# Kernel tuning notes

Measured on AMD Instinct MI355X. Metric: run time of the kernel, lower is better.

Reference implementation:

```python
import jax, jax.numpy as jnp
import numpy as np

N_NODES = 100000
N_EDGES = 800000
D = 64
N_ITERS = 3  # n_layers - 1


def setup_inputs() -> dict:
    key = jax.random.key(0)
    k1, k2, k3, k4 = jax.random.split(key, 4)
    x = jax.random.normal(k1, (N_NODES, D), dtype=jnp.float32)
    edge_index = jax.random.randint(k2, (2, N_EDGES), 0, N_NODES, dtype=jnp.int64)
    edge_weight = jax.random.uniform(k3, (N_EDGES,), dtype=jnp.float32)
    # Linear(64, 64) weight, scaled ~ kaiming so 3 stacked layers stay bounded
    W = jax.random.normal(k4, (D, D), dtype=jnp.float32) * (1.0 / np.sqrt(D))
    b = jnp.zeros((D,), dtype=jnp.float32)
    return {"x": x, "edge_index": edge_index, "edge_weight": edge_weight, "W": W, "b": b}


def reference(x, edge_index, edge_weight, W, b):
    # Faithful math of RPINetEncoder.forward: (n_layers-1) iterations of
    # LinearAggregation (weighted scatter-add message passing + shared Linear)
    # followed by ReLU. Dropout output is discarded in the original -> no-op.
    src = edge_index[0]
    dst = edge_index[1]
    n = x.shape[0]
    for _ in range(N_ITERS):
        msgs = edge_weight[:, None] * x[src]                      # [E, D] gather
        agg = jax.ops.segment_sum(msgs, dst, num_segments=n)      # [N, D] scatter-add
        x = jax.nn.relu(agg @ W.T + b)                            # shared linear + relu
    return x
```

## Files before the change

kernel.cpp:

```cpp
#include <hip/hip_runtime.h>
#include <hip/hip_bf16.h>

#define D 64
#define FP_SCALE 1048576.0f
#define FP_INV   (1.0f / 1048576.0f)

__global__ void hist_kernel(const int* __restrict__ dst, int* __restrict__ counts, int E) {
    int e = blockIdx.x * blockDim.x + threadIdx.x;
    if (e < E) atomicAdd(&counts[dst[e]], 1);
}

__global__ void alloc_kernel(int* __restrict__ counts_cursor, int2* __restrict__ seg,
                             int* __restrict__ total, int N) {
    int n = blockIdx.x * blockDim.x + threadIdx.x;
    if (n < N) {
        int c = counts_cursor[n];
        int s = atomicAdd(total, c);
        seg[n] = make_int2(s, c);
        counts_cursor[n] = s;
    }
}

__global__ void fill_kernel(const int* __restrict__ src, const int* __restrict__ dst,
                            const float* __restrict__ ew, int* __restrict__ cursor,
                            float2* __restrict__ perm, int E) {
    int e = blockIdx.x * blockDim.x + threadIdx.x;
    if (e < E) {
        int p = atomicAdd(&cursor[dst[e]], 1);
        perm[p] = make_float2(__int_as_float(src[e]), ew[e]);
    }
}

__global__ void gather_linear_kernel(const float* __restrict__ x,
                                     const float2* __restrict__ perm,
                                     const int2* __restrict__ seg,
                                     const float* __restrict__ W,
                                     const float* __restrict__ bias,
                                     float* __restrict__ out, int N) {
    __shared__ float Ws[D][D + 1];
    __shared__ float bs[D];
    int t = threadIdx.x;
    for (int i = t; i < D * D; i += 256) Ws[i >> 6][i & 63] = W[i];
    if (t < D) bs[t] = bias[t];
    __syncthreads();

    int wave = t >> 6;
    int lane = t & 63;
    int g = lane >> 4;
    int c = (lane & 15) << 2;
    int nwaves = gridDim.x * 4;
    for (int n = blockIdx.x * 4 + wave; n < N; n += nwaves) {
        int2 sc = seg[n];
        int st = sc.x, cnt = sc.y;
        int ix = 0, iy = 0, iz = 0, iw = 0;
        int k = g;
        for (; k + 4 < cnt; k += 8) {
            float2 m0 = perm[st + k];
            float2 m1 = perm[st + k + 4];
            int s0 = __float_as_int(m0.x);
            int s1 = __float_as_int(m1.x);
            float w0 = m0.y * FP_SCALE;
            float w1 = m1.y * FP_SCALE;
            float4 v0 = *reinterpret_cast<const float4*>(&x[(size_t)s0 * D + c]);
            float4 v1 = *reinterpret_cast<const float4*>(&x[(size_t)s1 * D + c]);
            ix += (int)(w0 * v0.x) + (int)(w1 * v1.x);
            iy += (int)(w0 * v0.y) + (int)(w1 * v1.y);
            iz += (int)(w0 * v0.z) + (int)(w1 * v1.z);
            iw += (int)(w0 * v0.w) + (int)(w1 * v1.w);
        }
        if (k < cnt) {
            float2 m0 = perm[st + k];
            int s0 = __float_as_int(m0.x);
            float w0 = m0.y * FP_SCALE;
            float4 v0 = *reinterpret_cast<const float4*>(&x[(size_t)s0 * D + c]);
            ix += (int)(w0 * v0.x);
            iy += (int)(w0 * v0.y);
            iz += (int)(w0 * v0.z);
            iw += (int)(w0 * v0.w);
        }
        #pragma unroll
        for (int mask = 16; mask <= 32; mask <<= 1) {
            ix += __shfl_xor(ix, mask);
            iy += __shfl_xor(iy, mask);
            iz += __shfl_xor(iz, mask);
            iw += __shfl_xor(iw, mask);
        }
        float ax = (float)ix * FP_INV;
        float ay = (float)iy * FP_INV;
        float az = (float)iz * FP_INV;
        float aw = (float)iw * FP_INV;
        float o = bs[lane];
        #pragma unroll
        for (int d = 0; d < D; ++d) {
            float comp = ((d & 3) == 0) ? ax : ((d & 3) == 1) ? ay : ((d & 3) == 2) ? az : aw;
            float a = __int_as_float(__builtin_amdgcn_readlane(__float_as_int(comp), d >> 2));
            o = fmaf(a, Ws[lane][d], o);
        }
        out[(size_t)n * D + lane] = fmaxf(o, 0.0f);
    }
}

__global__ void rpi_scatter_kernel(const float* __restrict__ x,
                                   const int* __restrict__ src,
                                   const int* __restrict__ dst,
                                   const float* __restrict__ ew,
                                   int* __restrict__ agg, int E) {
    int tid = blockIdx.x * blockDim.x + threadIdx.x;
    int e = tid >> 4;
    if (e >= E) return;
    int c = (tid & 15) << 2;
    int s = src[e], d = dst[e];
    float w = ew[e] * FP_SCALE;
    float4 v = *reinterpret_cast<const float4*>(&x[(size_t)s * D + c]);
    int* o = &agg[(size_t)d * D + c];
    atomicAdd(o + 0, (int)(w * v.x));
    atomicAdd(o + 1, (int)(w * v.y));
    atomicAdd(o + 2, (int)(w * v.z));
    atomicAdd(o + 3, (int)(w * v.w));
}

__global__ void rpi_linear_relu_kernel(const int* __restrict__ agg,
                                       const float* __restrict__ W,
                                       const float* __restrict__ b,
                                       float* __restrict__ out, int N) {
    __shared__ float Ws[D][D + 1];
    __shared__ float bs[D];
    int t = threadIdx.x;
    for (int i = t; i < D * D; i += 256) Ws[i >> 6][i & 63] = W[i];
    if (t < D) bs[t] = b[t];
    __syncthreads();
    int wave = t >> 6, lane = t & 63;
    int nwaves = gridDim.x * 4;
    for (int n = blockIdx.x * 4 + wave; n < N; n += nwaves) {
        const int* arow = &agg[(size_t)n * D];
        float acc = bs[lane];
        #pragma unroll
        for (int d = 0; d < D; ++d) acc = fmaf((float)arow[d] * FP_INV, Ws[lane][d], acc);
        out[(size_t)n * D + lane] = fmaxf(acc, 0.0f);
    }
}

extern "C" void kernel_launch(void* const* d_in, const int* in_sizes, int n_in,
                              void* d_out, int out_size, void* d_ws, size_t ws_size,
                              hipStream_t stream) {
    const float* x0 = (const float*)d_in[0];
    const int*   ei = (const int*)d_in[1];
    const float* ew = (const float*)d_in[2];
    const float* W  = (const float*)d_in[3];
    const float* b  = (const float*)d_in[4];
    float* out = (float*)d_out;

    int N = in_sizes[0] / D;
    int E = in_sizes[2];
    const int* src = ei;
    const int* dst = ei + E;

    size_t xbytes   = (size_t)N * D * sizeof(float);
    size_t intBytes = ((size_t)3 * N + 2) * sizeof(int);
    size_t need     = xbytes + intBytes + (size_t)E * sizeof(float2);

    if (ws_size >= need) {
        float*  xbuf   = (float*)d_ws;
        int2*   seg    = (int2*)((char*)d_ws + xbytes);
        int*    cursor = (int*)(seg + N);
        float2* perm   = (float2*)((char*)d_ws + xbytes + intBytes);
        int*    total  = cursor + N;

        hipMemsetAsync(cursor, 0, (size_t)(N + 2) * sizeof(int), stream);
        int eb = (E + 255) / 256;
        int nb = (N + 255) / 256;
        hist_kernel <<<eb, 256, 0, stream>>>(dst, cursor, E);
        alloc_kernel<<<nb, 256, 0, stream>>>(cursor, seg, total, N);
        fill_kernel <<<eb, 256, 0, stream>>>(src, dst, ew, cursor, perm, E);

        gather_linear_kernel<<<4096, 256, 0, stream>>>(x0,   perm, seg, W, b, out,  N);
        gather_linear_kernel<<<4096, 256, 0, stream>>>(out,  perm, seg, W, b, xbuf, N);
        gather_linear_kernel<<<4096, 256, 0, stream>>>(xbuf, perm, seg, W, b, out,  N);
    } else {
        int* agg = (int*)d_ws;
        const float* xcur = x0;
        int sb = (E * 16 + 255) / 256;
        for (int it = 0; it < 3; ++it) {
            hipMemsetAsync(agg, 0, xbytes, stream);
            rpi_scatter_kernel<<<sb, 256, 0, stream>>>(xcur, src, dst, ew, agg, E);
            rpi_linear_relu_kernel<<<2048, 256, 0, stream>>>(agg, W, b, out, N);
            xcur = out;
        }
    }
}
```

Baseline: 372.4 us.

## Store node features in bf16 for gathers and use a wave-scan CSR offset allocation

Converts the input features to bf16 and keeps the intermediate layer outputs in bf16, which halves the bytes read by the random gathers in each layer. Also pre-scales the edge weights when the CSR is filled, replaces the per-node atomic offset allocation with a wave prefix scan plus one atomic per wave, and splits the matvec accumulation into four independent chains. The cost is an extra conversion kernel, reduced feature precision, and a smaller fixed-point scale that shifts accumulation error.

```diff
diff --git a/kernel.cpp b/kernel.cpp
--- a/kernel.cpp
+++ b/kernel.cpp
@@ -2,8 +2,14 @@
 #include <hip/hip_bf16.h>
 
 #define D 64
-#define FP_SCALE 1048576.0f
-#define FP_INV   (1.0f / 1048576.0f)
+#define FP_SCALE 262144.0f
+#define FP_INV   (1.0f / 262144.0f)
+
+__device__ __forceinline__ unsigned short f2bf(float f) {
+    unsigned int u = __float_as_uint(f);
+    u += 0x7fffu + ((u >> 16) & 1u);
+    return (unsigned short)(u >> 16);
+}
 
 __global__ void hist_kernel(const int* __restrict__ dst, int* __restrict__ counts, int E) {
     int e = blockIdx.x * blockDim.x + threadIdx.x;
@@ -13,11 +19,22 @@
 __global__ void alloc_kernel(int* __restrict__ counts_cursor, int2* __restrict__ seg,
                              int* __restrict__ total, int N) {
     int n = blockIdx.x * blockDim.x + threadIdx.x;
+    int lane = threadIdx.x & 63;
+    int c = (n < N) ? counts_cursor[n] : 0;
+    int incl = c;
+    #pragma unroll
+    for (int off = 1; off < 64; off <<= 1) {
+        int t = __shfl_up(incl, off);
+        if (lane >= off) incl += t;
+    }
+    int wsum = __shfl(incl, 63);
+    int base = 0;
+    if (lane == 63) base = atomicAdd(total, wsum);
+    base = __shfl(base, 63);
     if (n < N) {
-        int c = counts_cursor[n];
-        int s = atomicAdd(total, c);
-        seg[n] = make_int2(s, c);
-        counts_cursor[n] = s;
+        int st = base + incl - c;
+        seg[n] = make_int2(st, c);
+        counts_cursor[n] = st;
     }
 }
 
@@ -27,16 +44,26 @@
     int e = blockIdx.x * blockDim.x + threadIdx.x;
     if (e < E) {
         int p = atomicAdd(&cursor[dst[e]], 1);
-        perm[p] = make_float2(__int_as_float(src[e]), ew[e]);
-    }
-}
-
-__global__ void gather_linear_kernel(const float* __restrict__ x,
+        perm[p] = make_float2(__int_as_float(src[e]), ew[e] * FP_SCALE);
+    }
+}
+
+__global__ void cvt_kernel(const float* __restrict__ in, unsigned short* __restrict__ out, int n4) {
+    int i = blockIdx.x * blockDim.x + threadIdx.x;
+    if (i >= n4) return;
+    float4 v = reinterpret_cast<const float4*>(in)[i];
+    ushort4 o;
+    o.x = f2bf(v.x); o.y = f2bf(v.y); o.z = f2bf(v.z); o.w = f2bf(v.w);
+    reinterpret_cast<ushort4*>(out)[i] = o;
+}
+
+template<bool OUT_BF>
+__global__ void gather_linear_kernel(const unsigned short* __restrict__ xb,
                                      const float2* __restrict__ perm,
                                      const int2* __restrict__ seg,
                                      const float* __restrict__ W,
                                      const float* __restrict__ bias,
-                                     float* __restrict__ out, int N) {
+                                     void* __restrict__ xout, int N) {
     __shared__ float Ws[D][D + 1];
     __shared__ float bs[D];
     int t = threadIdx.x;
@@ -59,24 +86,27 @@
             float2 m1 = perm[st + k + 4];
             int s0 = __float_as_int(m0.x);
             int s1 = __float_as_int(m1.x);
-            float w0 = m0.y * FP_SCALE;
-            float w1 = m1.y * FP_SCALE;
-            float4 v0 = *reinterpret_cast<const float4*>(&x[(size_t)s0 * D + c]);
-            float4 v1 = *reinterpret_cast<const float4*>(&x[(size_t)s1 * D + c]);
-            ix += (int)(w0 * v0.x) + (int)(w1 * v1.x);
-            iy += (int)(w0 * v0.y) + (int)(w1 * v1.y);
-            iz += (int)(w0 * v0.z) + (int)(w1 * v1.z);
-            iw += (int)(w0 * v0.w) + (int)(w1 * v1.w);
+            uint2 u0 = *reinterpret_cast<const uint2*>(&xb[(size_t)s0 * D + c]);
+            uint2 u1 = *reinterpret_cast<const uint2*>(&xb[(size_t)s1 * D + c]);
+            float w0 = m0.y, w1 = m1.y;
+            ix += (int)(w0 * __uint_as_float(u0.x << 16))
+                + (int)(w1 * __uint_as_float(u1.x << 16));
+            iy += (int)(w0 * __uint_as_float(u0.x & 0xffff0000u))
+                + (int)(w1 * __uint_as_float(u1.x & 0xffff0000u));
+            iz += (int)(w0 * __uint_as_float(u0.y << 16))
+                + (int)(w1 * __uint_as_float(u1.y << 16));
+            iw += (int)(w0 * __uint_as_float(u0.y & 0xffff0000u))
+                + (int)(w1 * __uint_as_float(u1.y & 0xffff0000u));
         }
         if (k < cnt) {
             float2 m0 = perm[st + k];
             int s0 = __float_as_int(m0.x);
-            float w0 = m0.y * FP_SCALE;
-            float4 v0 = *reinterpret_cast<const float4*>(&x[(size_t)s0 * D + c]);
-            ix += (int)(w0 * v0.x);
-            iy += (int)(w0 * v0.y);
-            iz += (int)(w0 * v0.z);
-            iw += (int)(w0 * v0.w);
+            uint2 u0 = *reinterpret_cast<const uint2*>(&xb[(size_t)s0 * D + c]);
+            float w0 = m0.y;
+            ix += (int)(w0 * __uint_as_float(u0.x << 16));
+            iy += (int)(w0 * __uint_as_float(u0.x & 0xffff0000u));
+            iz += (int)(w0 * __uint_as_float(u0.y << 16));
+            iw += (int)(w0 * __uint_as_float(u0.y & 0xffff0000u));
         }
         #pragma unroll
         for (int mask = 16; mask <= 32; mask <<= 1) {
@@ -89,14 +119,17 @@
         float ay = (float)iy * FP_INV;
         float az = (float)iz * FP_INV;
         float aw = (float)iw * FP_INV;
-        float o = bs[lane];
+        float o0 = 0.f, o1 = 0.f, o2 = 0.f, o3 = 0.f;
         #pragma unroll
-        for (int d = 0; d < D; ++d) {
-            float comp = ((d & 3) == 0) ? ax : ((d & 3) == 1) ? ay : ((d & 3) == 2) ? az : aw;
-            float a = __int_as_float(__builtin_amdgcn_readlane(__float_as_int(comp), d >> 2));
-            o = fmaf(a, Ws[lane][d], o);
-        }
-        out[(size_t)n * D + lane] = fmaxf(o, 0.0f);
+        for (int q = 0; q < 16; ++q) {
+            o0 = fmaf(__int_as_float(__builtin_amdgcn_readlane(__float_as_int(ax), q)), Ws[lane][4 * q + 0], o0);
+            o1 = fmaf(__int_as_float(__builtin_amdgcn_readlane(__float_as_int(ay), q)), Ws[lane][4 * q + 1], o1);
+            o2 = fmaf(__int_as_float(__builtin_amdgcn_readlane(__float_as_int(az), q)), Ws[lane][4 * q + 2], o2);
+            o3 = fmaf(__int_as_float(__builtin_amdgcn_readlane(__float_as_int(aw), q)), Ws[lane][4 * q + 3], o3);
+        }
+        float o = fmaxf(bs[lane] + ((o0 + o1) + (o2 + o3)), 0.0f);
+        if (OUT_BF) ((unsigned short*)xout)[(size_t)n * D + lane] = f2bf(o);
+        else        ((float*)xout)[(size_t)n * D + lane] = o;
     }
 }
 
@@ -155,33 +188,36 @@
     const int* src = ei;
     const int* dst = ei + E;
 
-    size_t xbytes   = (size_t)N * D * sizeof(float);
-    size_t intBytes = ((size_t)3 * N + 2) * sizeof(int);
-    size_t need     = xbytes + intBytes + (size_t)E * sizeof(float2);
+    size_t xeb      = (size_t)N * D * sizeof(unsigned short);
+    size_t intBytes = ((size_t)3 * N + 4) * sizeof(int);
+    size_t need     = 2 * xeb + intBytes + (size_t)E * sizeof(float2);
 
     if (ws_size >= need) {
-        float*  xbuf   = (float*)d_ws;
-        int2*   seg    = (int2*)((char*)d_ws + xbytes);
-        int*    cursor = (int*)(seg + N);
-        float2* perm   = (float2*)((char*)d_ws + xbytes + intBytes);
-        int*    total  = cursor + N;
+        unsigned short* xb1 = (unsigned short*)d_ws;
+        unsigned short* xb2 = xb1 + (size_t)N * D;
+        int2*  seg    = (int2*)((char*)d_ws + 2 * xeb);
+        int*   cursor = (int*)(seg + N);
+        int*   total  = cursor + N;
+        float2* perm  = (float2*)((char*)d_ws + 2 * xeb + intBytes);
 
         hipMemsetAsync(cursor, 0, (size_t)(N + 2) * sizeof(int), stream);
         int eb = (E + 255) / 256;
         int nb = (N + 255) / 256;
+        int n4 = N * D / 4;
         hist_kernel <<<eb, 256, 0, stream>>>(dst, cursor, E);
         alloc_kernel<<<nb, 256, 0, stream>>>(cursor, seg, total, N);
         fill_kernel <<<eb, 256, 0, stream>>>(src, dst, ew, cursor, perm, E);
-
-        gather_linear_kernel<<<4096, 256, 0, stream>>>(x0,   perm, seg, W, b, out,  N);
-        gather_linear_kernel<<<4096, 256, 0, stream>>>(out,  perm, seg, W, b, xbuf, N);
-        gather_linear_kernel<<<4096, 256, 0, stream>>>(xbuf, perm, seg, W, b, out,  N);
+        cvt_kernel  <<<(n4 + 255) / 256, 256, 0, stream>>>(x0, xb1, n4);
+
+        gather_linear_kernel<true> <<<4096, 256, 0, stream>>>(xb1, perm, seg, W, b, xb2, N);
+        gather_linear_kernel<true> <<<4096, 256, 0, stream>>>(xb2, perm, seg, W, b, xb1, N);
+        gather_linear_kernel<false><<<4096, 256, 0, stream>>>(xb1, perm, seg, W, b, out, N);
     } else {
         int* agg = (int*)d_ws;
         const float* xcur = x0;
         int sb = (E * 16 + 255) / 256;
         for (int it = 0; it < 3; ++it) {
-            hipMemsetAsync(agg, 0, xbytes, stream);
+            hipMemsetAsync(agg, 0, (size_t)N * D * sizeof(int), stream);
             rpi_scatter_kernel<<<sb, 256, 0, stream>>>(xcur, src, dst, ew, agg, E);
             rpi_linear_relu_kernel<<<2048, 256, 0, stream>>>(agg, W, b, out, N);
             xcur = out;
```

New measurement: 332.3 us. -10.8%, faster.
